# Kernel tuning notes

Measured on AMD Instinct MI355X. Metric: run time of the kernel, lower is better.

## Reference

```python
import jax, jax.numpy as jnp
import numpy as np

B, S, D, H = 2, 4096, 1024, 16
HD = D // H  # 64


def setup_inputs() -> dict:
    key = jax.random.key(0)
    ks = jax.random.split(key, 6)
    return {
        "x": jax.random.normal(ks[0], (B, S, D), dtype=jnp.float32),
        "mask": jax.random.normal(ks[1], (B, S, S), dtype=jnp.float32),
        "Wqkv": jax.random.normal(ks[2], (D, 3 * D), dtype=jnp.float32) * 0.02,
        "bqkv": jax.random.normal(ks[3], (3 * D,), dtype=jnp.float32) * 0.02,
        "Wo": jax.random.normal(ks[4], (D, D), dtype=jnp.float32) * 0.02,
        "bo": jax.random.normal(ks[5], (D,), dtype=jnp.float32) * 0.02,
    }


def reference(x, mask, Wqkv, bqkv, Wo, bo):
    b, s, d = x.shape
    # fused QKV projection: [B,S,3D]
    qkv = jnp.einsum('bsd,de->bse', x, Wqkv) + bqkv
    # [B,S,H,3*HD] -> [B,H,S,3*HD]
    qkv = qkv.reshape(b, s, H, 3 * HD).transpose(0, 2, 1, 3)
    q, k, v = jnp.split(qkv, 3, axis=-1)  # each [B,H,S,HD]
    scale = 1.0 / jnp.sqrt(jnp.asarray(HD, dtype=x.dtype))
    scores = jnp.einsum('bhqe,bhke->bhqk', q, k) * scale  # [B,H,S,S]
    scores = scores + mask[:, None, :, :]  # additive mask broadcast over heads
    attn = jax.nn.softmax(scores, axis=-1)
    values = jnp.einsum('bhqk,bhke->bhqe', attn, v)  # [B,H,S,HD]
    # NOTE: faithful to original TF code: reshape WITHOUT transposing heads back
    values = values.reshape(b, s, d)
    out = jnp.einsum('bsd,de->bse', values, Wo) + bo
    return out
```

## Files before the change

kernel.cpp:

```cpp
#include <hip/hip_runtime.h>
#include <hip/hip_bf16.h>

#define DEV __device__ __forceinline__

typedef unsigned short u16;
typedef __attribute__((ext_vector_type(4))) float f32x4;
typedef __attribute__((ext_vector_type(8))) short s16x8;

static constexpr int Bc = 2, Hc = 16, Sc = 4096, Dc = 1024, HDc = 64;

DEV u16 f2bf(float f) {
  unsigned x = __float_as_uint(f);
  x += 0x7FFFu + ((x >> 16) & 1u);
  return (u16)(x >> 16);
}
DEV float bf2f(u16 u) { return __uint_as_float(((unsigned)u) << 16); }

DEV unsigned cvtpk_bf16(float lo, float hi) {
  unsigned r;
  asm("v_cvt_pk_bf16_f32 %0, %1, %2" : "=v"(r) : "v"(lo), "v"(hi));
  return r;
}

DEV void gload_lds16(const void* g, void* l) {
  __builtin_amdgcn_global_load_lds((const __attribute__((address_space(1))) void*)g,
                                   (__attribute__((address_space(3))) void*)l, 16, 0, 0);
}

DEV f32x4 mfma16(s16x8 a, s16x8 b, f32x4 c) {
  return __builtin_amdgcn_mfma_f32_16x16x32_bf16(a, b, c, 0, 0, 0);
}

DEV f32x4 fzero4() { f32x4 v; v[0] = v[1] = v[2] = v[3] = 0.f; return v; }

#define LOG2E_F 1.44269504088896340736f
#define QSCALE_F (0.125f * LOG2E_F)
#define MBIAS_F (12.0f * LOG2E_F)

__global__ void cvt_f32_bf16(const float* __restrict__ in, u16* __restrict__ out, size_t n,
                             float scale, float bias) {
  size_t i = ((size_t)blockIdx.x * blockDim.x + threadIdx.x) * 4;
  size_t stride = (size_t)gridDim.x * blockDim.x * 4;
  for (; i < n; i += stride) {
    float4 v = *(const float4*)(in + i);
    u16 a = f2bf(fmaf(v.x, scale, bias)), b = f2bf(fmaf(v.y, scale, bias));
    u16 c = f2bf(fmaf(v.z, scale, bias)), d = f2bf(fmaf(v.w, scale, bias));
    *(ushort4*)(out + i) = make_ushort4(a, b, c, d);
  }
}

__global__ void transpose_cvt(const float* __restrict__ in, u16* __restrict__ out, int R, int C) {
  __shared__ u16 t[64][72];
  int nct = C >> 6;
  int tr = blockIdx.x / nct, tc = blockIdx.x % nct;
  int r0 = tr << 6, c0 = tc << 6;
  int lr = threadIdx.x >> 2;
  int lc0 = (threadIdx.x & 3) << 4;
  const float* src = in + (size_t)(r0 + lr) * C + c0 + lc0;
#pragma unroll
  for (int j = 0; j < 16; j += 4) {
    float4 v = *(const float4*)(src + j);
    t[lr][lc0 + j + 0] = f2bf(v.x);
    t[lr][lc0 + j + 1] = f2bf(v.y);
    t[lr][lc0 + j + 2] = f2bf(v.z);
    t[lr][lc0 + j + 3] = f2bf(v.w);
  }
  __syncthreads();
  u16* dst = out + (size_t)(c0 + lr) * R + r0 + lc0;
#pragma unroll
  for (int j = 0; j < 16; j += 4) {
    u16 a = t[lc0 + j + 0][lr], b = t[lc0 + j + 1][lr], c = t[lc0 + j + 2][lr], d = t[lc0 + j + 3][lr];
    *(ushort4*)(dst + j) = make_ushort4(a, b, c, d);
  }
}

template <int MODE>
__global__ __launch_bounds__(256, 2) void gemm128(
    const u16* __restrict__ A, const u16* __restrict__ BT, const float* __restrict__ bias,
    void* __restrict__ out0, u16* __restrict__ out1, u16* __restrict__ out2,
    int N, int K, int grid_n) {
  __shared__ u16 Al[128 * 64];
  __shared__ u16 Bl[128 * 64];
  int bid = blockIdx.x;
  int bn = bid % grid_n, bm = bid / grid_n;
  int m0 = bm * 128, n0 = bn * 128;
  int tid = threadIdx.x, lane = tid & 63, wid = tid >> 6;
  int wm = wid >> 1, wn = wid & 1;
  int fr = lane & 15, fg = lane >> 4;

  f32x4 acc[4][4];
#pragma unroll
  for (int mi = 0; mi < 4; ++mi)
#pragma unroll
    for (int ni = 0; ni < 4; ++ni) acc[mi][ni] = fzero4();

  for (int kt = 0; kt < K; kt += 64) {
    const u16* Ag = A + (size_t)m0 * K + kt;
    const u16* Bg = BT + (size_t)n0 * K + kt;
#pragma unroll
    for (int it = 0; it < 4; ++it) {
      int L = it * 4096 + wid * 1024 + lane * 16;
      int row = L >> 7;
      int sch = ((L >> 4) & 7) ^ (row & 7);
      gload_lds16(Ag + (size_t)row * K + sch * 8, (char*)Al + it * 4096 + wid * 1024);
      gload_lds16(Bg + (size_t)row * K + sch * 8, (char*)Bl + it * 4096 + wid * 1024);
    }
    __syncthreads();
#pragma unroll
    for (int c = 0; c < 2; ++c) {
      s16x8 af[4], bfr[4];
#pragma unroll
      for (int mi = 0; mi < 4; ++mi) {
        int row = wm * 64 + mi * 16 + fr;
        int ch = (c * 4 + fg) ^ (row & 7);
        af[mi] = *(const s16x8*)((const char*)Al + row * 128 + ch * 16);
      }
#pragma unroll
      for (int ni = 0; ni < 4; ++ni) {
        int row = wn * 64 + ni * 16 + fr;
        int ch = (c * 4 + fg) ^ (row & 7);
        bfr[ni] = *(const s16x8*)((const char*)Bl + row * 128 + ch * 16);
      }
#pragma unroll
      for (int mi = 0; mi < 4; ++mi)
#pragma unroll
        for (int ni = 0; ni < 4; ++ni) acc[mi][ni] = mfma16(af[mi], bfr[ni], acc[mi][ni]);
    }
    __syncthreads();
  }

  if constexpr (MODE == 0) {
    u16* qb = (u16*)out0;
    u16* kb = out1;
    u16* vT = out2;
#pragma unroll
    for (int ni = 0; ni < 4; ++ni) {
      int n = n0 + wn * 64 + ni * 16 + fr;
      float bv = bias[n];
      int h = n / 192;
      int c = n % 192;
      int part = c >> 6;
      int e = c & 63;
#pragma unroll
      for (int mi = 0; mi < 4; ++mi) {
        int m = m0 + wm * 64 + mi * 16 + fg * 4;
        int b = m >> 12;
        int s = m & 4095;
        size_t bh = (size_t)b * Hc + h;
        if (part == 2) {
          u16 a0 = f2bf(acc[mi][ni][0] + bv), a1 = f2bf(acc[mi][ni][1] + bv);
          u16 a2 = f2bf(acc[mi][ni][2] + bv), a3 = f2bf(acc[mi][ni][3] + bv);
          *(ushort4*)(vT + ((bh * HDc + e) * (size_t)Sc + s)) = make_ushort4(a0, a1, a2, a3);
        } else if (part == 0) {
          u16* dst = qb + ((bh * Sc + s) * (size_t)HDc + e);
#pragma unroll
          for (int r = 0; r < 4; ++r)
            dst[(size_t)r * HDc] = f2bf((acc[mi][ni][r] + bv) * QSCALE_F);
        } else {
          u16* dst = kb + ((bh * Sc + s) * (size_t)HDc + e);
#pragma unroll
          for (int r = 0; r < 4; ++r) dst[(size_t)r * HDc] = f2bf(acc[mi][ni][r] + bv);
        }
      }
    }
  } else {
    float* O = (float*)out0;
#pragma unroll
    for (int ni = 0; ni < 4; ++ni) {
      int n = n0 + wn * 64 + ni * 16 + fr;
      float bv = bias[n];
#pragma unroll
      for (int mi = 0; mi < 4; ++mi) {
        int m = m0 + wm * 64 + mi * 16 + fg * 4;
#pragma unroll
        for (int r = 0; r < 4; ++r) O[(size_t)(m + r) * N + n] = acc[mi][ni][r] + bv;
      }
    }
  }
}

template <int MB>
__global__ __launch_bounds__(256, 6) void attn_kernel(
    const u16* __restrict__ qb, const u16* __restrict__ kb, const u16* __restrict__ vT,
    const void* __restrict__ maskp, u16* __restrict__ vals) {
  __shared__ u16 Kl[64 * 64];
  __shared__ u16 Vl[64 * 64];
  __shared__ char Pl[4 * 16 * 144];

  int bid = blockIdx.x;
  int h = bid & 15, b = (bid >> 4) & 1, qt = bid >> 5;
  int tid = threadIdx.x;
  int lane = tid & 63, wid = tid >> 6;
  int fr = lane & 15, fg = lane >> 4;
  size_t bh = (size_t)b * Hc + h;
  int q0 = qt * 64;
  int q = q0 + wid * 16 + fr;

  const u16* Qrow = qb + ((bh * Sc) + q) * (size_t)HDc;
  s16x8 qa0 = *(const s16x8*)(Qrow + fg * 8);
  s16x8 qa1 = *(const s16x8*)(Qrow + 32 + fg * 8);

  f32x4 o[4];
#pragma unroll
  for (int ef = 0; ef < 4; ++ef) o[ef] = fzero4();
  float lrun = 0.f;

  const u16* Kg = kb + bh * (size_t)Sc * HDc;
  const u16* Vg = vT + bh * (size_t)HDc * Sc;
  char* pw = (char*)Pl + wid * 2304 + fr * 144;

  int L0 = wid * 1024 + lane * 16;
  int L1 = L0 + 4096;
  int row0 = L0 >> 7, row1 = L1 >> 7;
  int sch0 = ((L0 >> 4) & 7) ^ (row0 & 7);
  int sch1 = ((L1 >> 4) & 7) ^ (row1 & 7);
  const u16* KgS0 = Kg + (size_t)row0 * HDc + sch0 * 8;
  const u16* KgS1 = Kg + (size_t)row1 * HDc + sch1 * 8;
  const u16* VgS0 = Vg + (size_t)row0 * Sc + sch0 * 8;
  const u16* VgS1 = Vg + (size_t)row1 * Sc + sch1 * 8;
  char* KlD0 = (char*)Kl + L0;  char* KlD1 = (char*)Kl + L1;
  char* VlD0 = (char*)Vl + L0;  char* VlD1 = (char*)Vl + L1;

  int kroff0 = fr * 128 + ((fg ^ (fr & 7)) << 4);
  int kroff1 = fr * 128 + (((4 + fg) ^ (fr & 7)) << 4);

  const u16* mk_b = (const u16*)maskp + ((size_t)b * Sc + q) * Sc + fg * 4;
  const float* mk_f = (const float*)maskp + ((size_t)b * Sc + q) * Sc + fg * 4;

  constexpr int NT = Sc / 64;

  gload_lds16(KgS0, KlD0);
  gload_lds16(KgS1, KlD1);
  gload_lds16(VgS0, VlD0);
  gload_lds16(VgS1, VlD1);
  __syncthreads();

  for (int kt = 0; kt < NT; ++kt) {
    f32x4 sa[4];
    if (MB) {
#pragma unroll
      for (int f = 0; f < 4; ++f) {
        ushort4 m4 = *(const ushort4*)(mk_b + kt * 64 + f * 16);
        sa[f][0] = bf2f(m4.x); sa[f][1] = bf2f(m4.y);
        sa[f][2] = bf2f(m4.z); sa[f][3] = bf2f(m4.w);
      }
    } else {
#pragma unroll
      for (int f = 0; f < 4; ++f) {
        float4 mf = *(const float4*)(mk_f + kt * 64 + f * 16);
        sa[f][0] = fmaf(mf.x, LOG2E_F, -MBIAS_F);
        sa[f][1] = fmaf(mf.y, LOG2E_F, -MBIAS_F);
        sa[f][2] = fmaf(mf.z, LOG2E_F, -MBIAS_F);
        sa[f][3] = fmaf(mf.w, LOG2E_F, -MBIAS_F);
      }
    }

    __builtin_amdgcn_s_setprio(1);
#pragma unroll
    for (int f = 0; f < 4; ++f) {
      s16x8 kf = *(const s16x8*)((const char*)Kl + f * 2048 + kroff0);
      sa[f] = mfma16(kf, qa0, sa[f]);
    }
#pragma unroll
    for (int f = 0; f < 4; ++f) {
      s16x8 kf = *(const s16x8*)((const char*)Kl + f * 2048 + kroff1);
      sa[f] = mfma16(kf, qa1, sa[f]);
    }
    __builtin_amdgcn_s_setprio(0);

    __syncthreads();

    if (kt + 1 < NT) {
      gload_lds16(KgS0 + (size_t)(kt + 1) * 4096, KlD0);
      gload_lds16(KgS1 + (size_t)(kt + 1) * 4096, KlD1);
    }

    float p[4][4];
#pragma unroll
    for (int f = 0; f < 4; ++f) {
      float p0 = __builtin_amdgcn_exp2f(sa[f][0]);
      float p1 = __builtin_amdgcn_exp2f(sa[f][1]);
      float p2 = __builtin_amdgcn_exp2f(sa[f][2]);
      float p3 = __builtin_amdgcn_exp2f(sa[f][3]);
      p[f][0] = p0; p[f][1] = p1; p[f][2] = p2; p[f][3] = p3;
      lrun += (p0 + p1) + (p2 + p3);
    }

#pragma unroll
    for (int f = 0; f < 4; ++f) {
      uint2 pk;
      pk.x = cvtpk_bf16(p[f][0], p[f][1]);
      pk.y = cvtpk_bf16(p[f][2], p[f][3]);
      *(uint2*)(pw + f * 32 + fg * 8) = pk;
    }

    s16x8 pa0 = *(const s16x8*)(pw + fg * 16);
    s16x8 pa1 = *(const s16x8*)(pw + 64 + fg * 16);
    __builtin_amdgcn_s_setprio(1);
#pragma unroll
    for (int ef = 0; ef < 4; ++ef) {
      s16x8 vf = *(const s16x8*)((const char*)Vl + ef * 2048 + kroff0);
      o[ef] = mfma16(vf, pa0, o[ef]);
    }
#pragma unroll
    for (int ef = 0; ef < 4; ++ef) {
      s16x8 vf = *(const s16x8*)((const char*)Vl + ef * 2048 + kroff1);
      o[ef] = mfma16(vf, pa1, o[ef]);
    }
    __builtin_amdgcn_s_setprio(0);

    __syncthreads();

    if (kt + 1 < NT) {
      gload_lds16(VgS0 + (size_t)(kt + 1) * 64, VlD0);
      gload_lds16(VgS1 + (size_t)(kt + 1) * 64, VlD1);
    }
  }

  lrun += __shfl_xor(lrun, 16, 64);
  lrun += __shfl_xor(lrun, 32, 64);
  float inv = 1.f / lrun;

  u16* vbase = vals + (size_t)b * Sc * Dc + (size_t)h * Sc * HDc + (size_t)q * HDc;
#pragma unroll
  for (int ef = 0; ef < 4; ++ef) {
    ushort4 ov = make_ushort4(f2bf(o[ef][0] * inv), f2bf(o[ef][1] * inv),
                              f2bf(o[ef][2] * inv), f2bf(o[ef][3] * inv));
    *(ushort4*)(vbase + ef * 16 + fg * 4) = ov;
  }
}

extern "C" void kernel_launch(void* const* d_in, const int* in_sizes, int n_in,
                              void* d_out, int out_size, void* d_ws, size_t ws_size,
                              hipStream_t stream) {
  (void)in_sizes; (void)n_in; (void)out_size;
  const float* x    = (const float*)d_in[0];
  const float* mask = (const float*)d_in[1];
  const float* Wqkv = (const float*)d_in[2];
  const float* bqkv = (const float*)d_in[3];
  const float* Wo   = (const float*)d_in[4];
  const float* bo   = (const float*)d_in[5];
  float* out = (float*)d_out;
  char* ws = (char*)d_ws;

  u16* xb    = (u16*)(ws + 0);
  u16* wqkvT = (u16*)(ws + 16777216);
  u16* woT   = (u16*)(ws + 23068672);
  u16* qb    = (u16*)(ws + 25165824);
  u16* kb    = (u16*)(ws + 41943040);
  u16* vT    = (u16*)(ws + 58720256);
  u16* vals  = (u16*)(ws + 75497472);
  u16* maskb = (u16*)(ws + 92274688);
  int use_mb = (ws_size >= 159383552ull) ? 1 : 0;

  cvt_f32_bf16<<<dim3(2048), dim3(256), 0, stream>>>(x, xb, (size_t)8388608, 1.0f, 0.0f);
  if (use_mb)
    cvt_f32_bf16<<<dim3(4096), dim3(256), 0, stream>>>(mask, maskb, (size_t)33554432,
                                                       LOG2E_F, -MBIAS_F);
  transpose_cvt<<<dim3(768), dim3(256), 0, stream>>>(Wqkv, wqkvT, 1024, 3072);
  transpose_cvt<<<dim3(256), dim3(256), 0, stream>>>(Wo, woT, 1024, 1024);

  gemm128<0><<<dim3(1536), dim3(256), 0, stream>>>(xb, wqkvT, bqkv, (void*)qb, kb, vT,
                                                   3072, 1024, 24);
  if (use_mb)
    attn_kernel<1><<<dim3(2048), dim3(256), 0, stream>>>(qb, kb, vT, (const void*)maskb, vals);
  else
    attn_kernel<0><<<dim3(2048), dim3(256), 0, stream>>>(qb, kb, vT, (const void*)mask, vals);
  gemm128<1><<<dim3(512), dim3(256), 0, stream>>>(vals, woT, bo, (void*)out, nullptr, nullptr,
                                                  1024, 1024, 8);
}
```

Measured before the change: 440.4 us.

## Process two query tiles per attention block to reuse K/V tiles in LDS

Each attention workgroup now handles 128 query rows, as two 64-row sub-tiles A and B, instead of 64. Every K/V tile loaded into LDS is reused for both sub-tiles, and the grid is halved. This halves K/V global traffic and the number of barriers per unit of work, but it doubles accumulator registers, so occupancy is lowered from 6 to 5 waves and latency hiding may suffer. The shared P scratch buffer is reused sequentially for A and B within each wave.

```diff
diff --git a/kernel.cpp b/kernel.cpp
--- a/kernel.cpp
+++ b/kernel.cpp
@@ -180,7 +180,7 @@
 }
 
 template <int MB>
-__global__ __launch_bounds__(256, 6) void attn_kernel(
+__global__ __launch_bounds__(256, 5) void attn_kernel(
     const u16* __restrict__ qb, const u16* __restrict__ kb, const u16* __restrict__ vT,
     const void* __restrict__ maskp, u16* __restrict__ vals) {
   __shared__ u16 Kl[64 * 64];
@@ -193,17 +193,20 @@
   int lane = tid & 63, wid = tid >> 6;
   int fr = lane & 15, fg = lane >> 4;
   size_t bh = (size_t)b * Hc + h;
-  int q0 = qt * 64;
-  int q = q0 + wid * 16 + fr;
-
-  const u16* Qrow = qb + ((bh * Sc) + q) * (size_t)HDc;
-  s16x8 qa0 = *(const s16x8*)(Qrow + fg * 8);
-  s16x8 qa1 = *(const s16x8*)(Qrow + 32 + fg * 8);
-
-  f32x4 o[4];
-#pragma unroll
-  for (int ef = 0; ef < 4; ++ef) o[ef] = fzero4();
-  float lrun = 0.f;
+  int qA = qt * 128 + wid * 16 + fr;
+  int qB = qA + 64;
+
+  const u16* QrowA = qb + ((bh * Sc) + qA) * (size_t)HDc;
+  const u16* QrowB = qb + ((bh * Sc) + qB) * (size_t)HDc;
+  s16x8 qa0A = *(const s16x8*)(QrowA + fg * 8);
+  s16x8 qa1A = *(const s16x8*)(QrowA + 32 + fg * 8);
+  s16x8 qa0B = *(const s16x8*)(QrowB + fg * 8);
+  s16x8 qa1B = *(const s16x8*)(QrowB + 32 + fg * 8);
+
+  f32x4 oA[4], oB[4];
+#pragma unroll
+  for (int ef = 0; ef < 4; ++ef) { oA[ef] = fzero4(); oB[ef] = fzero4(); }
+  float lrunA = 0.f, lrunB = 0.f;
 
   const u16* Kg = kb + bh * (size_t)Sc * HDc;
   const u16* Vg = vT + bh * (size_t)HDc * Sc;
@@ -224,8 +227,10 @@
   int kroff0 = fr * 128 + ((fg ^ (fr & 7)) << 4);
   int kroff1 = fr * 128 + (((4 + fg) ^ (fr & 7)) << 4);
 
-  const u16* mk_b = (const u16*)maskp + ((size_t)b * Sc + q) * Sc + fg * 4;
-  const float* mk_f = (const float*)maskp + ((size_t)b * Sc + q) * Sc + fg * 4;
+  const u16* mkA_b = (const u16*)maskp + ((size_t)b * Sc + qA) * Sc + fg * 4;
+  const u16* mkB_b = (const u16*)maskp + ((size_t)b * Sc + qB) * Sc + fg * 4;
+  const float* mkA_f = (const float*)maskp + ((size_t)b * Sc + qA) * Sc + fg * 4;
+  const float* mkB_f = (const float*)maskp + ((size_t)b * Sc + qB) * Sc + fg * 4;
 
   constexpr int NT = Sc / 64;
 
@@ -236,22 +241,30 @@
   __syncthreads();
 
   for (int kt = 0; kt < NT; ++kt) {
-    f32x4 sa[4];
+    f32x4 saA[4], saB[4];
     if (MB) {
 #pragma unroll
       for (int f = 0; f < 4; ++f) {
-        ushort4 m4 = *(const ushort4*)(mk_b + kt * 64 + f * 16);
-        sa[f][0] = bf2f(m4.x); sa[f][1] = bf2f(m4.y);
-        sa[f][2] = bf2f(m4.z); sa[f][3] = bf2f(m4.w);
+        ushort4 mA = *(const ushort4*)(mkA_b + kt * 64 + f * 16);
+        ushort4 mB = *(const ushort4*)(mkB_b + kt * 64 + f * 16);
+        saA[f][0] = bf2f(mA.x); saA[f][1] = bf2f(mA.y);
+        saA[f][2] = bf2f(mA.z); saA[f][3] = bf2f(mA.w);
+        saB[f][0] = bf2f(mB.x); saB[f][1] = bf2f(mB.y);
+        saB[f][2] = bf2f(mB.z); saB[f][3] = bf2f(mB.w);
       }
     } else {
 #pragma unroll
       for (int f = 0; f < 4; ++f) {
-        float4 mf = *(const float4*)(mk_f + kt * 64 + f * 16);
-        sa[f][0] = fmaf(mf.x, LOG2E_F, -MBIAS_F);
-        sa[f][1] = fmaf(mf.y, LOG2E_F, -MBIAS_F);
-        sa[f][2] = fmaf(mf.z, LOG2E_F, -MBIAS_F);
-        sa[f][3] = fmaf(mf.w, LOG2E_F, -MBIAS_F);
+        float4 mA = *(const float4*)(mkA_f + kt * 64 + f * 16);
+        float4 mB = *(const float4*)(mkB_f + kt * 64 + f * 16);
+        saA[f][0] = fmaf(mA.x, LOG2E_F, -MBIAS_F);
+        saA[f][1] = fmaf(mA.y, LOG2E_F, -MBIAS_F);
+        saA[f][2] = fmaf(mA.z, LOG2E_F, -MBIAS_F);
+        saA[f][3] = fmaf(mA.w, LOG2E_F, -MBIAS_F);
+        saB[f][0] = fmaf(mB.x, LOG2E_F, -MBIAS_F);
+        saB[f][1] = fmaf(mB.y, LOG2E_F, -MBIAS_F);
+        saB[f][2] = fmaf(mB.z, LOG2E_F, -MBIAS_F);
+        saB[f][3] = fmaf(mB.w, LOG2E_F, -MBIAS_F);
       }
     }
 
@@ -259,12 +272,14 @@
 #pragma unroll
     for (int f = 0; f < 4; ++f) {
       s16x8 kf = *(const s16x8*)((const char*)Kl + f * 2048 + kroff0);
-      sa[f] = mfma16(kf, qa0, sa[f]);
+      saA[f] = mfma16(kf, qa0A, saA[f]);
+      saB[f] = mfma16(kf, qa0B, saB[f]);
     }
 #pragma unroll
     for (int f = 0; f < 4; ++f) {
       s16x8 kf = *(const s16x8*)((const char*)Kl + f * 2048 + kroff1);
-      sa[f] = mfma16(kf, qa1, sa[f]);
+      saA[f] = mfma16(kf, qa1A, saA[f]);
+      saB[f] = mfma16(kf, qa1B, saB[f]);
     }
     __builtin_amdgcn_s_setprio(0);
 
@@ -275,39 +290,73 @@
       gload_lds16(KgS1 + (size_t)(kt + 1) * 4096, KlD1);
     }
 
-    float p[4][4];
-#pragma unroll
-    for (int f = 0; f < 4; ++f) {
-      float p0 = __builtin_amdgcn_exp2f(sa[f][0]);
-      float p1 = __builtin_amdgcn_exp2f(sa[f][1]);
-      float p2 = __builtin_amdgcn_exp2f(sa[f][2]);
-      float p3 = __builtin_amdgcn_exp2f(sa[f][3]);
-      p[f][0] = p0; p[f][1] = p1; p[f][2] = p2; p[f][3] = p3;
-      lrun += (p0 + p1) + (p2 + p3);
-    }
-
+    float pA[4][4];
+#pragma unroll
+    for (int f = 0; f < 4; ++f) {
+      float p0 = __builtin_amdgcn_exp2f(saA[f][0]);
+      float p1 = __builtin_amdgcn_exp2f(saA[f][1]);
+      float p2 = __builtin_amdgcn_exp2f(saA[f][2]);
+      float p3 = __builtin_amdgcn_exp2f(saA[f][3]);
+      pA[f][0] = p0; pA[f][1] = p1; pA[f][2] = p2; pA[f][3] = p3;
+      lrunA += (p0 + p1) + (p2 + p3);
+    }
 #pragma unroll
     for (int f = 0; f < 4; ++f) {
       uint2 pk;
-      pk.x = cvtpk_bf16(p[f][0], p[f][1]);
-      pk.y = cvtpk_bf16(p[f][2], p[f][3]);
+      pk.x = cvtpk_bf16(pA[f][0], pA[f][1]);
+      pk.y = cvtpk_bf16(pA[f][2], pA[f][3]);
       *(uint2*)(pw + f * 32 + fg * 8) = pk;
     }
-
-    s16x8 pa0 = *(const s16x8*)(pw + fg * 16);
-    s16x8 pa1 = *(const s16x8*)(pw + 64 + fg * 16);
-    __builtin_amdgcn_s_setprio(1);
-#pragma unroll
-    for (int ef = 0; ef < 4; ++ef) {
-      s16x8 vf = *(const s16x8*)((const char*)Vl + ef * 2048 + kroff0);
-      o[ef] = mfma16(vf, pa0, o[ef]);
-    }
-#pragma unroll
-    for (int ef = 0; ef < 4; ++ef) {
-      s16x8 vf = *(const s16x8*)((const char*)Vl + ef * 2048 + kroff1);
-      o[ef] = mfma16(vf, pa1, o[ef]);
-    }
-    __builtin_amdgcn_s_setprio(0);
+    {
+      s16x8 pa0 = *(const s16x8*)(pw + fg * 16);
+      s16x8 pa1 = *(const s16x8*)(pw + 64 + fg * 16);
+      __builtin_amdgcn_s_setprio(1);
+#pragma unroll
+      for (int ef = 0; ef < 4; ++ef) {
+        s16x8 vf = *(const s16x8*)((const char*)Vl + ef * 2048 + kroff0);
+        oA[ef] = mfma16(vf, pa0, oA[ef]);
+      }
+#pragma unroll
+      for (int ef = 0; ef < 4; ++ef) {
+        s16x8 vf = *(const s16x8*)((const char*)Vl + ef * 2048 + kroff1);
+        oA[ef] = mfma16(vf, pa1, oA[ef]);
+      }
+      __builtin_amdgcn_s_setprio(0);
+    }
+
+    float pB[4][4];
+#pragma unroll
+    for (int f = 0; f < 4; ++f) {
+      float p0 = __builtin_amdgcn_exp2f(saB[f][0]);
+      float p1 = __builtin_amdgcn_exp2f(saB[f][1]);
+      float p2 = __builtin_amdgcn_exp2f(saB[f][2]);
+      float p3 = __builtin_amdgcn_exp2f(saB[f][3]);
+      pB[f][0] = p0; pB[f][1] = p1; pB[f][2] = p2; pB[f][3] = p3;
+      lrunB += (p0 + p1) + (p2 + p3);
+    }
+#pragma unroll
+    for (int f = 0; f < 4; ++f) {
+      uint2 pk;
+      pk.x = cvtpk_bf16(pB[f][0], pB[f][1]);
+      pk.y = cvtpk_bf16(pB[f][2], pB[f][3]);
+      *(uint2*)(pw + f * 32 + fg * 8) = pk;
+    }
+    {
+      s16x8 pa0 = *(const s16x8*)(pw + fg * 16);
+      s16x8 pa1 = *(const s16x8*)(pw + 64 + fg * 16);
+      __builtin_amdgcn_s_setprio(1);
+#pragma unroll
+      for (int ef = 0; ef < 4; ++ef) {
+        s16x8 vf = *(const s16x8*)((const char*)Vl + ef * 2048 + kroff0);
+        oB[ef] = mfma16(vf, pa0, oB[ef]);
+      }
+#pragma unroll
+      for (int ef = 0; ef < 4; ++ef) {
+        s16x8 vf = *(const s16x8*)((const char*)Vl + ef * 2048 + kroff1);
+        oB[ef] = mfma16(vf, pa1, oB[ef]);
+      }
+      __builtin_amdgcn_s_setprio(0);
+    }
 
     __syncthreads();
 
@@ -317,16 +366,23 @@
     }
   }
 
-  lrun += __shfl_xor(lrun, 16, 64);
-  lrun += __shfl_xor(lrun, 32, 64);
-  float inv = 1.f / lrun;
-
-  u16* vbase = vals + (size_t)b * Sc * Dc + (size_t)h * Sc * HDc + (size_t)q * HDc;
+  lrunA += __shfl_xor(lrunA, 16, 64);
+  lrunA += __shfl_xor(lrunA, 32, 64);
+  lrunB += __shfl_xor(lrunB, 16, 64);
+  lrunB += __shfl_xor(lrunB, 32, 64);
+  float invA = 1.f / lrunA;
+  float invB = 1.f / lrunB;
+
+  u16* vbaseA = vals + (size_t)b * Sc * Dc + (size_t)h * Sc * HDc + (size_t)qA * HDc;
+  u16* vbaseB = vals + (size_t)b * Sc * Dc + (size_t)h * Sc * HDc + (size_t)qB * HDc;
 #pragma unroll
   for (int ef = 0; ef < 4; ++ef) {
-    ushort4 ov = make_ushort4(f2bf(o[ef][0] * inv), f2bf(o[ef][1] * inv),
-                              f2bf(o[ef][2] * inv), f2bf(o[ef][3] * inv));
-    *(ushort4*)(vbase + ef * 16 + fg * 4) = ov;
+    ushort4 ovA = make_ushort4(f2bf(oA[ef][0] * invA), f2bf(oA[ef][1] * invA),
+                               f2bf(oA[ef][2] * invA), f2bf(oA[ef][3] * invA));
+    *(ushort4*)(vbaseA + ef * 16 + fg * 4) = ovA;
+    ushort4 ovB = make_ushort4(f2bf(oB[ef][0] * invB), f2bf(oB[ef][1] * invB),
+                               f2bf(oB[ef][2] * invB), f2bf(oB[ef][3] * invB));
+    *(ushort4*)(vbaseB + ef * 16 + fg * 4) = ovB;
   }
 }
 
@@ -363,9 +419,9 @@
   gemm128<0><<<dim3(1536), dim3(256), 0, stream>>>(xb, wqkvT, bqkv, (void*)qb, kb, vT,
                                                    3072, 1024, 24);
   if (use_mb)
-    attn_kernel<1><<<dim3(2048), dim3(256), 0, stream>>>(qb, kb, vT, (const void*)maskb, vals);
+    attn_kernel<1><<<dim3(1024), dim3(256), 0, stream>>>(qb, kb, vT, (const void*)maskb, vals);
   else
-    attn_kernel<0><<<dim3(2048), dim3(256), 0, stream>>>(qb, kb, vT, (const void*)mask, vals);
+    attn_kernel<0><<<dim3(1024), dim3(256), 0, stream>>>(qb, kb, vT, (const void*)mask, vals);
   gemm128<1><<<dim3(512), dim3(256), 0, stream>>>(vals, woT, bo, (void*)out, nullptr, nullptr,
                                                   1024, 1024, 8);
 }
```

Result: slower. 678.1 us (+54.0%).

## Double-buffer K/V tiles in LDS and prefetch mask one tile ahead

Applied to the files above, without the earlier changes.

Adds a second LDS buffer for the K and V tiles. The next tile's async global-to-LDS loads are issued at the top of each iteration, which drops one of the two per-iteration barriers. The mask values for the next tile are also loaded into registers one iteration early. The aim is to hide global memory latency behind the MFMA and exp work. In exchange, LDS use doubles, launch_bounds drops from 6 to 3 blocks per SM, and register pressure rises from the prefetched mask, all of which reduce occupancy.

```diff
diff --git a/kernel.cpp b/kernel.cpp
--- a/kernel.cpp
+++ b/kernel.cpp
@@ -180,11 +180,11 @@
 }
 
 template <int MB>
-__global__ __launch_bounds__(256, 6) void attn_kernel(
+__global__ __launch_bounds__(256, 3) void attn_kernel(
     const u16* __restrict__ qb, const u16* __restrict__ kb, const u16* __restrict__ vT,
     const void* __restrict__ maskp, u16* __restrict__ vals) {
-  __shared__ u16 Kl[64 * 64];
-  __shared__ u16 Vl[64 * 64];
+  __shared__ u16 Kl[2][64 * 64];
+  __shared__ u16 Vl[2][64 * 64];
   __shared__ char Pl[4 * 16 * 144];
 
   int bid = blockIdx.x;
@@ -193,8 +193,7 @@
   int lane = tid & 63, wid = tid >> 6;
   int fr = lane & 15, fg = lane >> 4;
   size_t bh = (size_t)b * Hc + h;
-  int q0 = qt * 64;
-  int q = q0 + wid * 16 + fr;
+  int q = qt * 64 + wid * 16 + fr;
 
   const u16* Qrow = qb + ((bh * Sc) + q) * (size_t)HDc;
   s16x8 qa0 = *(const s16x8*)(Qrow + fg * 8);
@@ -218,8 +217,6 @@
   const u16* KgS1 = Kg + (size_t)row1 * HDc + sch1 * 8;
   const u16* VgS0 = Vg + (size_t)row0 * Sc + sch0 * 8;
   const u16* VgS1 = Vg + (size_t)row1 * Sc + sch1 * 8;
-  char* KlD0 = (char*)Kl + L0;  char* KlD1 = (char*)Kl + L1;
-  char* VlD0 = (char*)Vl + L0;  char* VlD1 = (char*)Vl + L1;
 
   int kroff0 = fr * 128 + ((fg ^ (fr & 7)) << 4);
   int kroff1 = fr * 128 + (((4 + fg) ^ (fr & 7)) << 4);
@@ -229,51 +226,70 @@
 
   constexpr int NT = Sc / 64;
 
-  gload_lds16(KgS0, KlD0);
-  gload_lds16(KgS1, KlD1);
-  gload_lds16(VgS0, VlD0);
-  gload_lds16(VgS1, VlD1);
+  gload_lds16(KgS0, (char*)Kl[0] + L0);
+  gload_lds16(KgS1, (char*)Kl[0] + L1);
+  gload_lds16(VgS0, (char*)Vl[0] + L0);
+  gload_lds16(VgS1, (char*)Vl[0] + L1);
+  ushort4 mcur_b[4];
+  float4 mcur_f[4];
+  if (MB) {
+#pragma unroll
+    for (int f = 0; f < 4; ++f) mcur_b[f] = *(const ushort4*)(mk_b + f * 16);
+  } else {
+#pragma unroll
+    for (int f = 0; f < 4; ++f) mcur_f[f] = *(const float4*)(mk_f + f * 16);
+  }
   __syncthreads();
 
   for (int kt = 0; kt < NT; ++kt) {
+    int cur = kt & 1, nxt = cur ^ 1;
+
+    ushort4 mnx_b[4];
+    float4 mnx_f[4];
+    if (kt + 1 < NT) {
+      if (MB) {
+#pragma unroll
+        for (int f = 0; f < 4; ++f) mnx_b[f] = *(const ushort4*)(mk_b + (kt + 1) * 64 + f * 16);
+      } else {
+#pragma unroll
+        for (int f = 0; f < 4; ++f) mnx_f[f] = *(const float4*)(mk_f + (kt + 1) * 64 + f * 16);
+      }
+      gload_lds16(KgS0 + (size_t)(kt + 1) * 4096, (char*)Kl[nxt] + L0);
+      gload_lds16(KgS1 + (size_t)(kt + 1) * 4096, (char*)Kl[nxt] + L1);
+      gload_lds16(VgS0 + (size_t)(kt + 1) * 64, (char*)Vl[nxt] + L0);
+      gload_lds16(VgS1 + (size_t)(kt + 1) * 64, (char*)Vl[nxt] + L1);
+    }
+
     f32x4 sa[4];
     if (MB) {
 #pragma unroll
       for (int f = 0; f < 4; ++f) {
-        ushort4 m4 = *(const ushort4*)(mk_b + kt * 64 + f * 16);
-        sa[f][0] = bf2f(m4.x); sa[f][1] = bf2f(m4.y);
-        sa[f][2] = bf2f(m4.z); sa[f][3] = bf2f(m4.w);
+        sa[f][0] = bf2f(mcur_b[f].x); sa[f][1] = bf2f(mcur_b[f].y);
+        sa[f][2] = bf2f(mcur_b[f].z); sa[f][3] = bf2f(mcur_b[f].w);
       }
     } else {
 #pragma unroll
       for (int f = 0; f < 4; ++f) {
-        float4 mf = *(const float4*)(mk_f + kt * 64 + f * 16);
-        sa[f][0] = fmaf(mf.x, LOG2E_F, -MBIAS_F);
-        sa[f][1] = fmaf(mf.y, LOG2E_F, -MBIAS_F);
-        sa[f][2] = fmaf(mf.z, LOG2E_F, -MBIAS_F);
-        sa[f][3] = fmaf(mf.w, LOG2E_F, -MBIAS_F);
-      }
-    }
-
+        sa[f][0] = fmaf(mcur_f[f].x, LOG2E_F, -MBIAS_F);
+        sa[f][1] = fmaf(mcur_f[f].y, LOG2E_F, -MBIAS_F);
+        sa[f][2] = fmaf(mcur_f[f].z, LOG2E_F, -MBIAS_F);
+        sa[f][3] = fmaf(mcur_f[f].w, LOG2E_F, -MBIAS_F);
+      }
+    }
+
+    const char* Kc = (const char*)Kl[cur];
     __builtin_amdgcn_s_setprio(1);
 #pragma unroll
     for (int f = 0; f < 4; ++f) {
-      s16x8 kf = *(const s16x8*)((const char*)Kl + f * 2048 + kroff0);
+      s16x8 kf = *(const s16x8*)(Kc + f * 2048 + kroff0);
       sa[f] = mfma16(kf, qa0, sa[f]);
     }
 #pragma unroll
     for (int f = 0; f < 4; ++f) {
-      s16x8 kf = *(const s16x8*)((const char*)Kl + f * 2048 + kroff1);
+      s16x8 kf = *(const s16x8*)(Kc + f * 2048 + kroff1);
       sa[f] = mfma16(kf, qa1, sa[f]);
     }
     __builtin_amdgcn_s_setprio(0);
-
-    __syncthreads();
-
-    if (kt + 1 < NT) {
-      gload_lds16(KgS0 + (size_t)(kt + 1) * 4096, KlD0);
-      gload_lds16(KgS1 + (size_t)(kt + 1) * 4096, KlD1);
-    }
 
     float p[4][4];
 #pragma unroll
@@ -294,27 +310,33 @@
       *(uint2*)(pw + f * 32 + fg * 8) = pk;
     }
 
+    const char* Vc = (const char*)Vl[cur];
     s16x8 pa0 = *(const s16x8*)(pw + fg * 16);
     s16x8 pa1 = *(const s16x8*)(pw + 64 + fg * 16);
     __builtin_amdgcn_s_setprio(1);
 #pragma unroll
     for (int ef = 0; ef < 4; ++ef) {
-      s16x8 vf = *(const s16x8*)((const char*)Vl + ef * 2048 + kroff0);
+      s16x8 vf = *(const s16x8*)(Vc + ef * 2048 + kroff0);
       o[ef] = mfma16(vf, pa0, o[ef]);
     }
 #pragma unroll
     for (int ef = 0; ef < 4; ++ef) {
-      s16x8 vf = *(const s16x8*)((const char*)Vl + ef * 2048 + kroff1);
+      s16x8 vf = *(const s16x8*)(Vc + ef * 2048 + kroff1);
       o[ef] = mfma16(vf, pa1, o[ef]);
     }
     __builtin_amdgcn_s_setprio(0);
 
+    if (kt + 1 < NT) {
+      if (MB) {
+#pragma unroll
+        for (int f = 0; f < 4; ++f) mcur_b[f] = mnx_b[f];
+      } else {
+#pragma unroll
+        for (int f = 0; f < 4; ++f) mcur_f[f] = mnx_f[f];
+      }
+    }
+
     __syncthreads();
-
-    if (kt + 1 < NT) {
-      gload_lds16(VgS0 + (size_t)(kt + 1) * 64, VlD0);
-      gload_lds16(VgS1 + (size_t)(kt + 1) * 64, VlD1);
-    }
   }
 
   lrun += __shfl_xor(lrun, 16, 64);
```

Result: no change. 444.1 us (+0.8%).
